# Kernel optimization log

Measured on AMD Instinct MI355X. Metric: run time of the kernel, lower is better.

Reference implementation:

```python
import jax, jax.numpy as jnp
import numpy as np


def sobel_kernels_3d(dtype=jnp.float32):
    # Standard 3D Sobel: derivative [-1,0,1] along one axis, smoothing [1,2,1]
    # along the other two. Returns shape (3, 1, 3, 3, 3) in OIDHW layout.
    s = jnp.array([1.0, 2.0, 1.0], dtype=dtype)
    d = jnp.array([-1.0, 0.0, 1.0], dtype=dtype)
    kd = jnp.einsum('i,j,k->ijk', d, s, s)  # d/dD
    kh = jnp.einsum('i,j,k->ijk', s, d, s)  # d/dH
    kw = jnp.einsum('i,j,k->ijk', s, s, d)  # d/dW
    return jnp.stack([kd, kh, kw], axis=0)[:, None]  # (3,1,3,3,3)


def _grad3d(x, kernels):
    # x: (B, C, D, H, W) -> flatten (B*C, 1, D, H, W), conv with padding=1.
    B, C, D, H, W = x.shape
    x_ = x.reshape(B * C, 1, D, H, W)
    return jax.lax.conv_general_dilated(
        x_, kernels.astype(x.dtype),
        window_strides=(1, 1, 1),
        padding=((1, 1), (1, 1), (1, 1)),
        dimension_numbers=('NCDHW', 'OIDHW', 'NCDHW'),
    )  # (B*C, 3, D, H, W)


def setup_inputs() -> dict:
    key = jax.random.key(0)
    k1, k2 = jax.random.split(key)
    shape = (4, 4, 64, 128, 128)
    pred = jax.random.normal(k1, shape, dtype=jnp.float32)
    target = jax.random.normal(k2, shape, dtype=jnp.float32)
    return {"pred": pred, "target": target}


def reference(pred, target):
    kernels = sobel_kernels_3d(pred.dtype)
    grad_pred = _grad3d(pred, kernels)
    grad_target = _grad3d(target, kernels)
    # loss_type == 'l1'
    return jnp.mean(jnp.abs(grad_pred - grad_target))
```

## Files before the change

kernel.cpp:

```cpp
#include <hip/hip_runtime.h>

#define NB 16
#define DD 64
#define HH 128
#define WW 128
#define HW (HH * WW)

constexpr int TROWS = 16;
constexpr int NQ = 8;
constexpr int QP = DD / NQ;
constexpr float INV_COUNT = 1.0f / 50331648.0f;

__global__ void zero_out_kernel(float* out) {
    if (threadIdx.x == 0 && blockIdx.x == 0) out[0] = 0.0f;
}


#define ROWPART(D0, D1, LM, RP, RSa, RSb, RWa, RWb)                         \
    RSa.x = (LM)   + 2.f*D0.x + D0.y;  RSa.y = D0.x + 2.f*D0.y + D0.z;      \
    RSa.z = D0.y + 2.f*D0.z + D0.w;    RSa.w = D0.z + 2.f*D0.w + D1.x;      \
    RSb.x = D0.w + 2.f*D1.x + D1.y;    RSb.y = D1.x + 2.f*D1.y + D1.z;      \
    RSb.z = D1.y + 2.f*D1.z + D1.w;    RSb.w = D1.z + 2.f*D1.w + (RP);      \
    RWa.x = D0.y - (LM);   RWa.y = D0.z - D0.x;                             \
    RWa.z = D0.w - D0.y;   RWa.w = D1.x - D0.z;                             \
    RWb.x = D1.y - D0.w;   RWb.y = D1.z - D1.x;                             \
    RWb.z = D1.w - D1.y;   RWb.w = (RP) - D1.z;

#define DIFF4(D, A, B, F)                                                   \
    D.x = (A.x - B.x) * (F); D.y = (A.y - B.y) * (F);                       \
    D.z = (A.z - B.z) * (F); D.w = (A.w - B.w) * (F);

#define PARTIALS(...) PARTIALS_IMPL(__VA_ARGS__)
#define PARTIALS_IMPL(REL, MD, Aa, Ab, Ha, Hb, Wa, Wb) do {                 \
    const int pc_ = min(max(d0 + (REL), 0), DD - 1);                        \
    const float* pp_ = pred   + nbase + (size_t)pc_ * HW;                   \
    const float* pt_ = target + nbase + (size_t)pc_ * HW;                   \
    const float4 am0_ = *(const float4*)(pp_ + ro_m);                       \
    const float4 am1_ = *(const float4*)(pp_ + ro_m + 4);                   \
    const float4 a00_ = *(const float4*)(pp_ + ro_0);                       \
    const float4 a01_ = *(const float4*)(pp_ + ro_0 + 4);                   \
    const float4 ap0_ = *(const float4*)(pp_ + ro_p);                       \
    const float4 ap1_ = *(const float4*)(pp_ + ro_p + 4);                   \
    const float4 bm0_ = *(const float4*)(pt_ + ro_m);                       \
    const float4 bm1_ = *(const float4*)(pt_ + ro_m + 4);                   \
    const float4 b00_ = *(const float4*)(pt_ + ro_0);                       \
    const float4 b01_ = *(const float4*)(pt_ + ro_0 + 4);                   \
    const float4 bp0_ = *(const float4*)(pt_ + ro_p);                       \
    const float4 bp1_ = *(const float4*)(pt_ + ro_p + 4);                   \
    const float fm_ = mr_m * (MD), f0_ = (MD), fp_ = mr_p * (MD);           \
    float4 dm0_, dm1_, d00_, d01_, dp0_, dp1_;                              \
    DIFF4(dm0_, am0_, bm0_, fm_) DIFF4(dm1_, am1_, bm1_, fm_)               \
    DIFF4(d00_, a00_, b00_, f0_) DIFF4(d01_, a01_, b01_, f0_)               \
    DIFF4(dp0_, ap0_, bp0_, fp_) DIFF4(dp1_, ap1_, bp1_, fp_)               \
    const float lmm_ = __shfl_up(dm1_.w, 1, 16) * lmask;                    \
    const float rpm_ = __shfl_down(dm0_.x, 1, 16) * rmask;                  \
    const float lm0_ = __shfl_up(d01_.w, 1, 16) * lmask;                    \
    const float rp0_ = __shfl_down(d00_.x, 1, 16) * rmask;                  \
    const float lmp_ = __shfl_up(dp1_.w, 1, 16) * lmask;                    \
    const float rpp_ = __shfl_down(dp0_.x, 1, 16) * rmask;                  \
    float4 sma_, smb_, wma_, wmb_;                                          \
    float4 s0a_, s0b_, w0a_, w0b_;                                          \
    float4 spa_, spb_, wpa_, wpb_;                                          \
    ROWPART(dm0_, dm1_, lmm_, rpm_, sma_, smb_, wma_, wmb_)                 \
    ROWPART(d00_, d01_, lm0_, rp0_, s0a_, s0b_, w0a_, w0b_)                 \
    ROWPART(dp0_, dp1_, lmp_, rpp_, spa_, spb_, wpa_, wpb_)                 \
    Aa.x = sma_.x + 2.f*s0a_.x + spa_.x;  Aa.y = sma_.y + 2.f*s0a_.y + spa_.y; \
    Aa.z = sma_.z + 2.f*s0a_.z + spa_.z;  Aa.w = sma_.w + 2.f*s0a_.w + spa_.w; \
    Ab.x = smb_.x + 2.f*s0b_.x + spb_.x;  Ab.y = smb_.y + 2.f*s0b_.y + spb_.y; \
    Ab.z = smb_.z + 2.f*s0b_.z + spb_.z;  Ab.w = smb_.w + 2.f*s0b_.w + spb_.w; \
    Ha.x = spa_.x - sma_.x;  Ha.y = spa_.y - sma_.y;                        \
    Ha.z = spa_.z - sma_.z;  Ha.w = spa_.w - sma_.w;                        \
    Hb.x = spb_.x - smb_.x;  Hb.y = spb_.y - smb_.y;                        \
    Hb.z = spb_.z - smb_.z;  Hb.w = spb_.w - smb_.w;                        \
    Wa.x = wma_.x + 2.f*w0a_.x + wpa_.x;  Wa.y = wma_.y + 2.f*w0a_.y + wpa_.y; \
    Wa.z = wma_.z + 2.f*w0a_.z + wpa_.z;  Wa.w = wma_.w + 2.f*w0a_.w + wpa_.w; \
    Wb.x = wmb_.x + 2.f*w0b_.x + wpb_.x;  Wb.y = wmb_.y + 2.f*w0b_.y + wpb_.y; \
    Wb.z = wmb_.z + 2.f*w0b_.z + wpb_.z;  Wb.w = wmb_.w + 2.f*w0b_.w + wpb_.w; \
} while (0)

#define EMIT(...) EMIT_IMPL(__VA_ARGS__)
#define EMIT_IMPL(A0a,A0b,H0a,H0b,W0a,W0b, A1a,A1b,H1a,H1b,W1a,W1b, A2a,A2b,H2a,H2b,W2a,W2b) do { \
    acc += fabsf(A2a.x - A0a.x) + fabsf(A2a.y - A0a.y)                      \
         + fabsf(A2a.z - A0a.z) + fabsf(A2a.w - A0a.w);                     \
    acc += fabsf(A2b.x - A0b.x) + fabsf(A2b.y - A0b.y)                      \
         + fabsf(A2b.z - A0b.z) + fabsf(A2b.w - A0b.w);                     \
    acc += fabsf(H0a.x + 2.f*H1a.x + H2a.x) + fabsf(H0a.y + 2.f*H1a.y + H2a.y) \
         + fabsf(H0a.z + 2.f*H1a.z + H2a.z) + fabsf(H0a.w + 2.f*H1a.w + H2a.w); \
    acc += fabsf(H0b.x + 2.f*H1b.x + H2b.x) + fabsf(H0b.y + 2.f*H1b.y + H2b.y) \
         + fabsf(H0b.z + 2.f*H1b.z + H2b.z) + fabsf(H0b.w + 2.f*H1b.w + H2b.w); \
    acc += fabsf(W0a.x + 2.f*W1a.x + W2a.x) + fabsf(W0a.y + 2.f*W1a.y + W2a.y) \
         + fabsf(W0a.z + 2.f*W1a.z + W2a.z) + fabsf(W0a.w + 2.f*W1a.w + W2a.w); \
    acc += fabsf(W0b.x + 2.f*W1b.x + W2b.x) + fabsf(W0b.y + 2.f*W1b.y + W2b.y) \
         + fabsf(W0b.z + 2.f*W1b.z + W2b.z) + fabsf(W0b.w + 2.f*W1b.w + W2b.w); \
} while (0)

#define SLOT0 c0Aa,c0Ab,c0Ha,c0Hb,c0Wa,c0Wb
#define SLOT1 c1Aa,c1Ab,c1Ha,c1Hb,c1Wa,c1Wb
#define SLOT2 c2Aa,c2Ab,c2Ha,c2Hb,c2Wa,c2Wb

__global__ __launch_bounds__(256) void sobel_l1_kernel(
    const float* __restrict__ pred,
    const float* __restrict__ target,
    float* __restrict__ out)
{
    __shared__ float wsum[4];

    const int tid = threadIdx.x;
    int b = blockIdx.x;
    const int bh = b & 7;  b >>= 3;
    const int q  = b & 7;  b >>= 3;
    const int bn = b;

    const int row = tid >> 4;
    const int sc  = tid & 15;
    const int gh  = bh * TROWS + row;
    const int d0  = q * QP;
    const size_t nbase = (size_t)bn * (size_t)(DD * HW);

    const int wq   = sc * 8;
    const int ro_m = max(gh - 1, 0) * WW + wq;
    const int ro_0 = gh * WW + wq;
    const int ro_p = min(gh + 1, HH - 1) * WW + wq;
    const float mr_m = (gh - 1 >= 0) ? 1.f : 0.f;
    const float mr_p = (gh + 1 < HH) ? 1.f : 0.f;
    const float lmask = (sc == 0)  ? 0.f : 1.f;
    const float rmask = (sc == 15) ? 0.f : 1.f;
    const float mdA = (q == 0)      ? 0.f : 1.f;
    const float mdB = (q == NQ - 1) ? 0.f : 1.f;

    float acc = 0.f;

    float4 c0Aa, c0Ab, c0Ha, c0Hb, c0Wa, c0Wb;
    float4 c1Aa, c1Ab, c1Ha, c1Hb, c1Wa, c1Wb;
    float4 c2Aa, c2Ab, c2Ha, c2Hb, c2Wa, c2Wb;

    PARTIALS(-1, mdA, SLOT0);
    PARTIALS( 0, 1.f, SLOT1);
    PARTIALS( 1, 1.f, SLOT2);  EMIT(SLOT0, SLOT1, SLOT2);
    PARTIALS( 2, 1.f, SLOT0);  EMIT(SLOT1, SLOT2, SLOT0);
    PARTIALS( 3, 1.f, SLOT1);  EMIT(SLOT2, SLOT0, SLOT1);
    PARTIALS( 4, 1.f, SLOT2);  EMIT(SLOT0, SLOT1, SLOT2);
    PARTIALS( 5, 1.f, SLOT0);  EMIT(SLOT1, SLOT2, SLOT0);
    PARTIALS( 6, 1.f, SLOT1);  EMIT(SLOT2, SLOT0, SLOT1);
    PARTIALS( 7, 1.f, SLOT2);  EMIT(SLOT0, SLOT1, SLOT2);
    PARTIALS( 8, mdB, SLOT0);  EMIT(SLOT1, SLOT2, SLOT0);

#pragma unroll
    for (int off = 32; off > 0; off >>= 1)
        acc += __shfl_down(acc, off, 64);
    if ((tid & 63) == 0) wsum[tid >> 6] = acc;
    __syncthreads();
    if (tid == 0) {
        const float s = wsum[0] + wsum[1] + wsum[2] + wsum[3];
        atomicAdd(out, s * INV_COUNT);
    }
}

extern "C" void kernel_launch(void* const* d_in, const int* in_sizes, int n_in,
                              void* d_out, int out_size, void* d_ws, size_t ws_size,
                              hipStream_t stream) {
    const float* pred   = (const float*)d_in[0];
    const float* target = (const float*)d_in[1];
    float* out = (float*)d_out;

    zero_out_kernel<<<1, 64, 0, stream>>>(out);

    const int nblocks = NB * NQ * (HH / TROWS);
    sobel_l1_kernel<<<nblocks, 256, 0, stream>>>(pred, target, out);
}
```

Baseline: 156.7 us.

## Double-buffer plane loads and carry running depth partials with narrower per-thread tiles

Each thread now handles 4 columns instead of 8, with 32 threads per row and 8 rows per block, so the grid doubles and launch_bounds asks for 4 blocks per CU. Loads for the next depth plane go into a second register set while the current plane is computed, so memory latency can overlap with arithmetic. The depth-direction combination keeps running partial sums (Ap1/Ap2, Hs/Hp, Ws/Wp) instead of three full slots, which lowers register pressure. The cost is more halo re-reads per output and more shuffles, since each thread now covers fewer columns.

Result: no change. 159.8 us (+2.0%).

```diff
diff --git a/kernel.cpp b/kernel.cpp
--- a/kernel.cpp
+++ b/kernel.cpp
@@ -6,7 +6,7 @@
 #define WW 128
 #define HW (HH * WW)
 
-constexpr int TROWS = 16;
+constexpr int TROWS = 8;
 constexpr int NQ = 8;
 constexpr int QP = DD / NQ;
 constexpr float INV_COUNT = 1.0f / 50331648.0f;
@@ -16,89 +16,72 @@
 }
 
 
-#define ROWPART(D0, D1, LM, RP, RSa, RSb, RWa, RWb)                         \
-    RSa.x = (LM)   + 2.f*D0.x + D0.y;  RSa.y = D0.x + 2.f*D0.y + D0.z;      \
-    RSa.z = D0.y + 2.f*D0.z + D0.w;    RSa.w = D0.z + 2.f*D0.w + D1.x;      \
-    RSb.x = D0.w + 2.f*D1.x + D1.y;    RSb.y = D1.x + 2.f*D1.y + D1.z;      \
-    RSb.z = D1.y + 2.f*D1.z + D1.w;    RSb.w = D1.z + 2.f*D1.w + (RP);      \
-    RWa.x = D0.y - (LM);   RWa.y = D0.z - D0.x;                             \
-    RWa.z = D0.w - D0.y;   RWa.w = D1.x - D0.z;                             \
-    RWb.x = D1.y - D0.w;   RWb.y = D1.z - D1.x;                             \
-    RWb.z = D1.w - D1.y;   RWb.w = (RP) - D1.z;
-
 #define DIFF4(D, A, B, F)                                                   \
     D.x = (A.x - B.x) * (F); D.y = (A.y - B.y) * (F);                       \
     D.z = (A.z - B.z) * (F); D.w = (A.w - B.w) * (F);
 
-#define PARTIALS(...) PARTIALS_IMPL(__VA_ARGS__)
-#define PARTIALS_IMPL(REL, MD, Aa, Ab, Ha, Hb, Wa, Wb) do {                 \
+#define ROWPART(D, LM, RP, RS, RW)                                          \
+    RS.x = (LM) + 2.f*D.x + D.y;   RS.y = D.x + 2.f*D.y + D.z;              \
+    RS.z = D.y + 2.f*D.z + D.w;    RS.w = D.z + 2.f*D.w + (RP);             \
+    RW.x = D.y - (LM);  RW.y = D.z - D.x;                                   \
+    RW.z = D.w - D.y;   RW.w = (RP) - D.z;
+
+#define RSET_A pAm, pA0, pAp, tAm, tA0, tAp
+#define RSET_B pBm, pB0, pBp, tBm, tB0, tBp
+
+#define PLOAD(...) PLOAD_I(__VA_ARGS__)
+#define PLOAD_I(Pm, P0, Pp, Tm, T0, Tp, REL) do {                           \
     const int pc_ = min(max(d0 + (REL), 0), DD - 1);                        \
     const float* pp_ = pred   + nbase + (size_t)pc_ * HW;                   \
     const float* pt_ = target + nbase + (size_t)pc_ * HW;                   \
-    const float4 am0_ = *(const float4*)(pp_ + ro_m);                       \
-    const float4 am1_ = *(const float4*)(pp_ + ro_m + 4);                   \
-    const float4 a00_ = *(const float4*)(pp_ + ro_0);                       \
-    const float4 a01_ = *(const float4*)(pp_ + ro_0 + 4);                   \
-    const float4 ap0_ = *(const float4*)(pp_ + ro_p);                       \
-    const float4 ap1_ = *(const float4*)(pp_ + ro_p + 4);                   \
-    const float4 bm0_ = *(const float4*)(pt_ + ro_m);                       \
-    const float4 bm1_ = *(const float4*)(pt_ + ro_m + 4);                   \
-    const float4 b00_ = *(const float4*)(pt_ + ro_0);                       \
-    const float4 b01_ = *(const float4*)(pt_ + ro_0 + 4);                   \
-    const float4 bp0_ = *(const float4*)(pt_ + ro_p);                       \
-    const float4 bp1_ = *(const float4*)(pt_ + ro_p + 4);                   \
-    const float fm_ = mr_m * (MD), f0_ = (MD), fp_ = mr_p * (MD);           \
-    float4 dm0_, dm1_, d00_, d01_, dp0_, dp1_;                              \
-    DIFF4(dm0_, am0_, bm0_, fm_) DIFF4(dm1_, am1_, bm1_, fm_)               \
-    DIFF4(d00_, a00_, b00_, f0_) DIFF4(d01_, a01_, b01_, f0_)               \
-    DIFF4(dp0_, ap0_, bp0_, fp_) DIFF4(dp1_, ap1_, bp1_, fp_)               \
-    const float lmm_ = __shfl_up(dm1_.w, 1, 16) * lmask;                    \
-    const float rpm_ = __shfl_down(dm0_.x, 1, 16) * rmask;                  \
-    const float lm0_ = __shfl_up(d01_.w, 1, 16) * lmask;                    \
-    const float rp0_ = __shfl_down(d00_.x, 1, 16) * rmask;                  \
-    const float lmp_ = __shfl_up(dp1_.w, 1, 16) * lmask;                    \
-    const float rpp_ = __shfl_down(dp0_.x, 1, 16) * rmask;                  \
-    float4 sma_, smb_, wma_, wmb_;                                          \
-    float4 s0a_, s0b_, w0a_, w0b_;                                          \
-    float4 spa_, spb_, wpa_, wpb_;                                          \
-    ROWPART(dm0_, dm1_, lmm_, rpm_, sma_, smb_, wma_, wmb_)                 \
-    ROWPART(d00_, d01_, lm0_, rp0_, s0a_, s0b_, w0a_, w0b_)                 \
-    ROWPART(dp0_, dp1_, lmp_, rpp_, spa_, spb_, wpa_, wpb_)                 \
-    Aa.x = sma_.x + 2.f*s0a_.x + spa_.x;  Aa.y = sma_.y + 2.f*s0a_.y + spa_.y; \
-    Aa.z = sma_.z + 2.f*s0a_.z + spa_.z;  Aa.w = sma_.w + 2.f*s0a_.w + spa_.w; \
-    Ab.x = smb_.x + 2.f*s0b_.x + spb_.x;  Ab.y = smb_.y + 2.f*s0b_.y + spb_.y; \
-    Ab.z = smb_.z + 2.f*s0b_.z + spb_.z;  Ab.w = smb_.w + 2.f*s0b_.w + spb_.w; \
-    Ha.x = spa_.x - sma_.x;  Ha.y = spa_.y - sma_.y;                        \
-    Ha.z = spa_.z - sma_.z;  Ha.w = spa_.w - sma_.w;                        \
-    Hb.x = spb_.x - smb_.x;  Hb.y = spb_.y - smb_.y;                        \
-    Hb.z = spb_.z - smb_.z;  Hb.w = spb_.w - smb_.w;                        \
-    Wa.x = wma_.x + 2.f*w0a_.x + wpa_.x;  Wa.y = wma_.y + 2.f*w0a_.y + wpa_.y; \
-    Wa.z = wma_.z + 2.f*w0a_.z + wpa_.z;  Wa.w = wma_.w + 2.f*w0a_.w + wpa_.w; \
-    Wb.x = wmb_.x + 2.f*w0b_.x + wpb_.x;  Wb.y = wmb_.y + 2.f*w0b_.y + wpb_.y; \
-    Wb.z = wmb_.z + 2.f*w0b_.z + wpb_.z;  Wb.w = wmb_.w + 2.f*w0b_.w + wpb_.w; \
+    Pm = *(const float4*)(pp_ + ro_m);                                      \
+    P0 = *(const float4*)(pp_ + ro_0);                                      \
+    Pp = *(const float4*)(pp_ + ro_p);                                      \
+    Tm = *(const float4*)(pt_ + ro_m);                                      \
+    T0 = *(const float4*)(pt_ + ro_0);                                      \
+    Tp = *(const float4*)(pt_ + ro_p);                                      \
 } while (0)
 
-#define EMIT(...) EMIT_IMPL(__VA_ARGS__)
-#define EMIT_IMPL(A0a,A0b,H0a,H0b,W0a,W0b, A1a,A1b,H1a,H1b,W1a,W1b, A2a,A2b,H2a,H2b,W2a,W2b) do { \
-    acc += fabsf(A2a.x - A0a.x) + fabsf(A2a.y - A0a.y)                      \
-         + fabsf(A2a.z - A0a.z) + fabsf(A2a.w - A0a.w);                     \
-    acc += fabsf(A2b.x - A0b.x) + fabsf(A2b.y - A0b.y)                      \
-         + fabsf(A2b.z - A0b.z) + fabsf(A2b.w - A0b.w);                     \
-    acc += fabsf(H0a.x + 2.f*H1a.x + H2a.x) + fabsf(H0a.y + 2.f*H1a.y + H2a.y) \
-         + fabsf(H0a.z + 2.f*H1a.z + H2a.z) + fabsf(H0a.w + 2.f*H1a.w + H2a.w); \
-    acc += fabsf(H0b.x + 2.f*H1b.x + H2b.x) + fabsf(H0b.y + 2.f*H1b.y + H2b.y) \
-         + fabsf(H0b.z + 2.f*H1b.z + H2b.z) + fabsf(H0b.w + 2.f*H1b.w + H2b.w); \
-    acc += fabsf(W0a.x + 2.f*W1a.x + W2a.x) + fabsf(W0a.y + 2.f*W1a.y + W2a.y) \
-         + fabsf(W0a.z + 2.f*W1a.z + W2a.z) + fabsf(W0a.w + 2.f*W1a.w + W2a.w); \
-    acc += fabsf(W0b.x + 2.f*W1b.x + W2b.x) + fabsf(W0b.y + 2.f*W1b.y + W2b.y) \
-         + fabsf(W0b.z + 2.f*W1b.z + W2b.z) + fabsf(W0b.w + 2.f*W1b.w + W2b.w); \
+#define PCOMP(...) PCOMP_I(__VA_ARGS__)
+#define PCOMP_I(Pm, P0, Pp, Tm, T0, Tp, MD, DOEMIT) do {                    \
+    const float fm_ = mr_m * (MD), f0_ = (MD), fp_ = mr_p * (MD);           \
+    float4 dm_, dc_, dp_;                                                   \
+    DIFF4(dm_, Pm, Tm, fm_)  DIFF4(dc_, P0, T0, f0_)  DIFF4(dp_, Pp, Tp, fp_) \
+    const float lmm_ = __shfl_up(dm_.w, 1, 32) * lmask;                     \
+    const float rpm_ = __shfl_down(dm_.x, 1, 32) * rmask;                   \
+    const float lmc_ = __shfl_up(dc_.w, 1, 32) * lmask;                     \
+    const float rpc_ = __shfl_down(dc_.x, 1, 32) * rmask;                   \
+    const float lmp_ = __shfl_up(dp_.w, 1, 32) * lmask;                     \
+    const float rpp_ = __shfl_down(dp_.x, 1, 32) * rmask;                   \
+    float4 sm_, sc_, sp_, wm_, wc_, wp_;                                    \
+    ROWPART(dm_, lmm_, rpm_, sm_, wm_)                                      \
+    ROWPART(dc_, lmc_, rpc_, sc_, wc_)                                      \
+    ROWPART(dp_, lmp_, rpp_, sp_, wp_)                                      \
+    float4 An_, Hn_, Wn_;                                                   \
+    An_.x = sm_.x + 2.f*sc_.x + sp_.x;  An_.y = sm_.y + 2.f*sc_.y + sp_.y;  \
+    An_.z = sm_.z + 2.f*sc_.z + sp_.z;  An_.w = sm_.w + 2.f*sc_.w + sp_.w;  \
+    Hn_.x = sp_.x - sm_.x;  Hn_.y = sp_.y - sm_.y;                          \
+    Hn_.z = sp_.z - sm_.z;  Hn_.w = sp_.w - sm_.w;                          \
+    Wn_.x = wm_.x + 2.f*wc_.x + wp_.x;  Wn_.y = wm_.y + 2.f*wc_.y + wp_.y;  \
+    Wn_.z = wm_.z + 2.f*wc_.z + wp_.z;  Wn_.w = wm_.w + 2.f*wc_.w + wp_.w;  \
+    if (DOEMIT) {                                                           \
+        acc += fabsf(An_.x - Ap2.x) + fabsf(An_.y - Ap2.y)                  \
+             + fabsf(An_.z - Ap2.z) + fabsf(An_.w - Ap2.w);                 \
+        acc += fabsf(Hs.x + Hn_.x) + fabsf(Hs.y + Hn_.y)                    \
+             + fabsf(Hs.z + Hn_.z) + fabsf(Hs.w + Hn_.w);                   \
+        acc += fabsf(Ws.x + Wn_.x) + fabsf(Ws.y + Wn_.y)                    \
+             + fabsf(Ws.z + Wn_.z) + fabsf(Ws.w + Wn_.w);                   \
+    }                                                                       \
+    Ap2 = Ap1;  Ap1 = An_;                                                  \
+    Hs.x = Hp.x + 2.f*Hn_.x;  Hs.y = Hp.y + 2.f*Hn_.y;                      \
+    Hs.z = Hp.z + 2.f*Hn_.z;  Hs.w = Hp.w + 2.f*Hn_.w;                      \
+    Hp = Hn_;                                                               \
+    Ws.x = Wp.x + 2.f*Wn_.x;  Ws.y = Wp.y + 2.f*Wn_.y;                      \
+    Ws.z = Wp.z + 2.f*Wn_.z;  Ws.w = Wp.w + 2.f*Wn_.w;                      \
+    Wp = Wn_;                                                               \
 } while (0)
 
-#define SLOT0 c0Aa,c0Ab,c0Ha,c0Hb,c0Wa,c0Wb
-#define SLOT1 c1Aa,c1Ab,c1Ha,c1Hb,c1Wa,c1Wb
-#define SLOT2 c2Aa,c2Ab,c2Ha,c2Hb,c2Wa,c2Wb
-
-__global__ __launch_bounds__(256) void sobel_l1_kernel(
+__global__ __launch_bounds__(256, 4) void sobel_l1_kernel(
     const float* __restrict__ pred,
     const float* __restrict__ target,
     float* __restrict__ out)
@@ -107,43 +90,53 @@
 
     const int tid = threadIdx.x;
     int b = blockIdx.x;
-    const int bh = b & 7;  b >>= 3;
+    const int bh = b & 15; b >>= 4;
     const int q  = b & 7;  b >>= 3;
     const int bn = b;
 
-    const int row = tid >> 4;
-    const int sc  = tid & 15;
+    const int row = tid >> 5;
+    const int sc  = tid & 31;
     const int gh  = bh * TROWS + row;
     const int d0  = q * QP;
     const size_t nbase = (size_t)bn * (size_t)(DD * HW);
 
-    const int wq   = sc * 8;
+    const int wq   = sc * 4;
     const int ro_m = max(gh - 1, 0) * WW + wq;
     const int ro_0 = gh * WW + wq;
     const int ro_p = min(gh + 1, HH - 1) * WW + wq;
-    const float mr_m = (gh - 1 >= 0) ? 1.f : 0.f;
+    const float mr_m = (gh >= 1) ? 1.f : 0.f;
     const float mr_p = (gh + 1 < HH) ? 1.f : 0.f;
     const float lmask = (sc == 0)  ? 0.f : 1.f;
-    const float rmask = (sc == 15) ? 0.f : 1.f;
+    const float rmask = (sc == 31) ? 0.f : 1.f;
     const float mdA = (q == 0)      ? 0.f : 1.f;
     const float mdB = (q == NQ - 1) ? 0.f : 1.f;
 
+    float4 pAm, pA0, pAp, tAm, tA0, tAp;
+    float4 pBm, pB0, pBp, tBm, tB0, tBp;
+    const float4 z4 = float4{0.f, 0.f, 0.f, 0.f};
+    float4 Ap1 = z4, Ap2 = z4, Hs = z4, Hp = z4, Ws = z4, Wp = z4;
     float acc = 0.f;
 
-    float4 c0Aa, c0Ab, c0Ha, c0Hb, c0Wa, c0Wb;
-    float4 c1Aa, c1Ab, c1Ha, c1Hb, c1Wa, c1Wb;
-    float4 c2Aa, c2Ab, c2Ha, c2Hb, c2Wa, c2Wb;
-
-    PARTIALS(-1, mdA, SLOT0);
-    PARTIALS( 0, 1.f, SLOT1);
-    PARTIALS( 1, 1.f, SLOT2);  EMIT(SLOT0, SLOT1, SLOT2);
-    PARTIALS( 2, 1.f, SLOT0);  EMIT(SLOT1, SLOT2, SLOT0);
-    PARTIALS( 3, 1.f, SLOT1);  EMIT(SLOT2, SLOT0, SLOT1);
-    PARTIALS( 4, 1.f, SLOT2);  EMIT(SLOT0, SLOT1, SLOT2);
-    PARTIALS( 5, 1.f, SLOT0);  EMIT(SLOT1, SLOT2, SLOT0);
-    PARTIALS( 6, 1.f, SLOT1);  EMIT(SLOT2, SLOT0, SLOT1);
-    PARTIALS( 7, 1.f, SLOT2);  EMIT(SLOT0, SLOT1, SLOT2);
-    PARTIALS( 8, mdB, SLOT0);  EMIT(SLOT1, SLOT2, SLOT0);
+    PLOAD(RSET_A, -1);
+    PLOAD(RSET_B,  0);
+    PCOMP(RSET_A, mdA, false);
+    PLOAD(RSET_A,  1);
+    PCOMP(RSET_B, 1.f, false);
+    PLOAD(RSET_B,  2);
+    PCOMP(RSET_A, 1.f, true);
+    PLOAD(RSET_A,  3);
+    PCOMP(RSET_B, 1.f, true);
+    PLOAD(RSET_B,  4);
+    PCOMP(RSET_A, 1.f, true);
+    PLOAD(RSET_A,  5);
+    PCOMP(RSET_B, 1.f, true);
+    PLOAD(RSET_B,  6);
+    PCOMP(RSET_A, 1.f, true);
+    PLOAD(RSET_A,  7);
+    PCOMP(RSET_B, 1.f, true);
+    PLOAD(RSET_B,  8);
+    PCOMP(RSET_A, 1.f, true);
+    PCOMP(RSET_B, mdB, true);
 
 #pragma unroll
     for (int off = 32; off > 0; off >>= 1)
```
